# Kernel tuning notes

Hardware: AMD Instinct MI355X
Metric: run time of the kernel (lower is better)

## Reference

```python
import jax, jax.numpy as jnp
import numpy as np
import math

D_MODEL = 1024
NUM_HEADS = 16
HEAD_DIM = D_MODEL // NUM_HEADS


def setup_inputs() -> dict:
    key = jax.random.key(0)
    ks = jax.random.split(key, 9)
    B, S = 2, 2048
    scale = 1.0 / math.sqrt(D_MODEL)
    x = jax.random.normal(ks[0], (B, S, D_MODEL), dtype=jnp.float32)
    # torch nn.Linear params: weight [out, in], bias [out]
    Wq = jax.random.normal(ks[1], (D_MODEL, D_MODEL), dtype=jnp.float32) * scale
    bq = jax.random.normal(ks[2], (D_MODEL,), dtype=jnp.float32) * scale
    Wk = jax.random.normal(ks[3], (D_MODEL, D_MODEL), dtype=jnp.float32) * scale
    bk = jax.random.normal(ks[4], (D_MODEL,), dtype=jnp.float32) * scale
    Wv = jax.random.normal(ks[5], (D_MODEL, D_MODEL), dtype=jnp.float32) * scale
    bv = jax.random.normal(ks[6], (D_MODEL,), dtype=jnp.float32) * scale
    Wo = jax.random.normal(ks[7], (D_MODEL, D_MODEL), dtype=jnp.float32) * scale
    bo = jax.random.normal(ks[8], (D_MODEL,), dtype=jnp.float32) * scale
    return {"x": x, "Wq": Wq, "bq": bq, "Wk": Wk, "bk": bk,
            "Wv": Wv, "bv": bv, "Wo": Wo, "bo": bo}


def reference(x, Wq, bq, Wk, bk, Wv, bv, Wo, bo):
    B, S, _ = x.shape
    H, Dh = NUM_HEADS, HEAD_DIM

    def proj(W, b):
        # torch Linear: x @ W.T + b -> [B,S,D] -> [B,H,S,Dh]
        y = jnp.einsum('bsd,ed->bse', x, W) + b
        return y.reshape(B, S, H, Dh).transpose(0, 2, 1, 3)

    Q = proj(Wq, bq)
    K = proj(Wk, bk)
    V = proj(Wv, bv)

    # scores [B,H,S,S], causal mask with -inf, then scale by 1/sqrt(head_dim)
    scores = jnp.einsum('bhqd,bhkd->bhqk', Q, K)
    causal = jnp.tril(jnp.ones((S, S), dtype=bool))
    scores = jnp.where(causal, scores, -jnp.inf)
    A = jax.nn.softmax(scores / math.sqrt(Dh), axis=-1)

    O = jnp.einsum('bhqk,bhkd->bhqd', A, V)  # [B,H,S,Dh]
    O = O.transpose(0, 2, 1, 3).reshape(B, S, H * Dh)
    return jnp.einsum('bsd,ed->bse', O, Wo) + bo
```

## Files before the change

### kernel.cpp

```cpp
#include <hip/hip_runtime.h>


typedef _Float16 f16x8 __attribute__((ext_vector_type(8)));
typedef _Float16 f16x4 __attribute__((ext_vector_type(4)));
typedef _Float16 f16x2 __attribute__((ext_vector_type(2)));
typedef float f32x4 __attribute__((ext_vector_type(4)));

#define S_  2048
#define DM  1024
#define NH  16
#define DH  64

__device__ __forceinline__ void gload_lds16(const void* g, void* s) {
  __builtin_amdgcn_global_load_lds(
      (const __attribute__((address_space(1))) void*)g,
      (__attribute__((address_space(3))) void*)s, 16, 0, 0);
}

__device__ __forceinline__ f16x2 pkrtz(float a, float b) {
  return __builtin_bit_cast(f16x2, __builtin_amdgcn_cvt_pkrtz(a, b));
}


__global__ void cvt_x_kernel(const float* __restrict__ src,
                             _Float16* __restrict__ dst) {
  const int i = blockIdx.x * 256 + threadIdx.x;
  const float4 v = ((const float4*)src)[i];
  f16x4 h;
  h[0] = (_Float16)v.x; h[1] = (_Float16)v.y;
  h[2] = (_Float16)v.z; h[3] = (_Float16)v.w;
  ((f16x4*)dst)[i] = h;
}

__global__ void cvt_w_kernel(const float* __restrict__ w0,
                             const float* __restrict__ w1,
                             const float* __restrict__ w2,
                             const float* __restrict__ w3,
                             _Float16* __restrict__ dst) {
  const int y = blockIdx.y;
  const float* src = (y == 0) ? w0 : (y == 1) ? w1 : (y == 2) ? w2 : w3;
  const int i = blockIdx.x * 256 + threadIdx.x;
  const float4 v = ((const float4*)src)[i];
  f16x4 h;
  h[0] = (_Float16)v.x; h[1] = (_Float16)v.y;
  h[2] = (_Float16)v.z; h[3] = (_Float16)v.w;
  ((f16x4*)(dst + (size_t)y * (DM * DM)))[i] = h;
}


__global__ __launch_bounds__(256, 2) void gemm_qkv_kernel(
    const _Float16* __restrict__ xb, const _Float16* __restrict__ wb,
    const float* __restrict__ bq, const float* __restrict__ bk,
    const float* __restrict__ bv, _Float16* __restrict__ qkv)
{
  __shared__ _Float16 As[2][128 * 32];
  __shared__ _Float16 Ws[2][128 * 32];
  const int z = blockIdx.z;
  const _Float16* W = wb + (size_t)z * (DM * DM);
  const float* bias = (z == 0) ? bq : ((z == 1) ? bk : bv);
  _Float16* out = qkv + (size_t)z * 4194304;

  const f32x4 z4 = {0.f, 0.f, 0.f, 0.f};
  f32x4 acc[4][4];
#pragma unroll
  for (int mi = 0; mi < 4; ++mi)
#pragma unroll
    for (int ni = 0; ni < 4; ++ni) acc[mi][ni] = z4;

  const int m0 = blockIdx.y * 128, n0 = blockIdx.x * 128;
  const int t = threadIdx.x;
  const int w = t >> 6, l = t & 63;
  const int quad = l >> 4, ln = l & 15;
  const int wm = (w >> 1) << 6, wn = (w & 1) << 6;
  const int srow = l >> 2, scol = (l & 3) << 3;

  for (int k0 = 0; k0 < DM; k0 += 64) {
#pragma unroll
    for (int h = 0; h < 2; ++h)
#pragma unroll
      for (int i = 0; i < 2; ++i) {
        const int ra = w * 32 + i * 16;
        gload_lds16(&xb[(size_t)(m0 + ra + srow) * DM + k0 + h * 32 + scol],
                    &As[h][ra * 32]);
        gload_lds16(&W[(size_t)(n0 + ra + srow) * DM + k0 + h * 32 + scol],
                    &Ws[h][ra * 32]);
      }
    __syncthreads();

#pragma unroll
    for (int h = 0; h < 2; ++h) {
      f16x8 af[4], bf[4];
#pragma unroll
      for (int mi = 0; mi < 4; ++mi)
        af[mi] = *(const f16x8*)&As[h][(wm + mi * 16 + ln) * 32 + quad * 8];
#pragma unroll
      for (int ni = 0; ni < 4; ++ni)
        bf[ni] = *(const f16x8*)&Ws[h][(wn + ni * 16 + ln) * 32 + quad * 8];
#pragma unroll
      for (int mi = 0; mi < 4; ++mi)
#pragma unroll
        for (int ni = 0; ni < 4; ++ni)
          acc[mi][ni] = __builtin_amdgcn_mfma_f32_16x16x32_f16(
              af[mi], bf[ni], acc[mi][ni], 0, 0, 0);
    }
    __syncthreads();
  }

  const float scale = (z == 0) ? 0.18033688f : 1.0f;

#pragma unroll
  for (int ni = 0; ni < 4; ++ni) {
    const int c = n0 + wn + ni * 16 + ln;
    const float bias_c = bias[c];
    const int h = c >> 6, d = c & 63;
#pragma unroll
    for (int mi = 0; mi < 4; ++mi) {
      const int mb = m0 + wm + mi * 16 + quad * 4;
#pragma unroll
      for (int r = 0; r < 4; ++r) {
        const int mg = mb + r;
        const int b = mg >> 11, s = mg & 2047;
        const int bh = b * NH + h;
        const float v = (acc[mi][ni][r] + bias_c) * scale;
        size_t idx;
        if (z == 2)
          idx = (size_t)bh * 131072 + (s >> 5) * 2048 + (d >> 4) * 512 +
                ((s >> 3) & 3) * 128 + (d & 15) * 8 + (s & 7);
        else
          idx = (size_t)bh * 131072 + (s >> 4) * 1024 + (d >> 5) * 512 +
                ((d >> 3) & 3) * 128 + (s & 15) * 8 + (d & 7);
        out[idx] = (_Float16)v;
      }
    }
  }
}


__global__ __launch_bounds__(256, 2) void gemm_out_kernel(
    const _Float16* __restrict__ ob, const _Float16* __restrict__ wo,
    const float* __restrict__ bo, float* __restrict__ out)
{
  __shared__ _Float16 As[128 * 32];
  __shared__ _Float16 Ws[64 * 32];
  const f32x4 z4 = {0.f, 0.f, 0.f, 0.f};
  f32x4 acc[2][4];
#pragma unroll
  for (int mi = 0; mi < 2; ++mi)
#pragma unroll
    for (int ni = 0; ni < 4; ++ni) acc[mi][ni] = z4;

  const int m0 = blockIdx.y * 128, n0 = blockIdx.x * 64;
  const int t = threadIdx.x;
  const int w = t >> 6, l = t & 63;
  const int quad = l >> 4, ln = l & 15;
  const int srow = l >> 2, scol = (l & 3) << 3;

  for (int k0 = 0; k0 < DM; k0 += 32) {
#pragma unroll
    for (int i = 0; i < 2; ++i) {
      const int ra = w * 32 + i * 16;
      gload_lds16(&ob[(size_t)(m0 + ra + srow) * DM + k0 + scol], &As[ra * 32]);
    }
    gload_lds16(&wo[(size_t)(n0 + w * 16 + srow) * DM + k0 + scol],
                &Ws[w * 16 * 32]);
    __syncthreads();

    f16x8 af[2], bf[4];
#pragma unroll
    for (int mi = 0; mi < 2; ++mi)
      af[mi] = *(const f16x8*)&As[(w * 32 + mi * 16 + ln) * 32 + quad * 8];
#pragma unroll
    for (int ni = 0; ni < 4; ++ni)
      bf[ni] = *(const f16x8*)&Ws[(ni * 16 + ln) * 32 + quad * 8];
#pragma unroll
    for (int mi = 0; mi < 2; ++mi)
#pragma unroll
      for (int ni = 0; ni < 4; ++ni)
        acc[mi][ni] = __builtin_amdgcn_mfma_f32_16x16x32_f16(
            af[mi], bf[ni], acc[mi][ni], 0, 0, 0);
    __syncthreads();
  }

#pragma unroll
  for (int ni = 0; ni < 4; ++ni) {
    const int c = n0 + ni * 16 + ln;
    const float bias_c = bo[c];
#pragma unroll
    for (int mi = 0; mi < 2; ++mi) {
      const int mb = m0 + w * 32 + mi * 16 + quad * 4;
#pragma unroll
      for (int r = 0; r < 4; ++r)
        out[(size_t)(mb + r) * DM + c] = acc[mi][ni][r] + bias_c;
    }
  }
}


template <bool DIAG>
__device__ __forceinline__ void compute_tile(
    const _Float16* __restrict__ kb_, const _Float16* __restrict__ vb_,
    int t, const f16x8 (&qf)[2][2], f32x4 (&oacc)[4][2],
    float (&l_i)[2], _Float16* Ps, int quad, int ln, int l)
{
  f16x8 kf[4], vf[4];
#pragma unroll
  for (int i = 0; i < 4; ++i)
    kf[i] = *(const f16x8*)(kb_ + (size_t)(t * 4 + i) * 512 + l * 8);
#pragma unroll
  for (int i = 0; i < 4; ++i)
    vf[i] = *(const f16x8*)(vb_ + (size_t)(t * 4 + i) * 512 + l * 8);

  const f32x4 z4 = {0.f, 0.f, 0.f, 0.f};
  f32x4 sacc[2][2];
#pragma unroll
  for (int mi = 0; mi < 2; ++mi)
#pragma unroll
    for (int qc = 0; qc < 2; ++qc) sacc[mi][qc] = z4;

#pragma unroll
  for (int ks = 0; ks < 2; ++ks)
#pragma unroll
    for (int mi = 0; mi < 2; ++mi)
#pragma unroll
      for (int qc = 0; qc < 2; ++qc)
        sacc[mi][qc] = __builtin_amdgcn_mfma_f32_16x16x32_f16(
            kf[mi * 2 + ks], qf[qc][ks], sacc[mi][qc], 0, 0, 0);

  const int sw = (ln & 3) << 1;
#pragma unroll
  for (int qc = 0; qc < 2; ++qc) {
    float rs = 0.f;
#pragma unroll
    for (int mi = 0; mi < 2; ++mi) {
      float p[4];
#pragma unroll
      for (int r = 0; r < 4; ++r) {
        p[r] = __builtin_amdgcn_exp2f(sacc[mi][qc][r]);
        if (DIAG && (mi * 16 + quad * 4 + r > qc * 16 + ln)) p[r] = 0.f;
        rs += p[r];
      }
      const f16x2 lo = pkrtz(p[0], p[1]);
      const f16x2 hi = pkrtz(p[2], p[3]);
      const f16x4 pk = __builtin_shufflevector(lo, hi, 0, 1, 2, 3);
      const int g = (mi * 4 + quad) ^ sw;
      *(f16x4*)&Ps[(qc * 16 + ln) * 40 + g * 4] = pk;
    }
    l_i[qc] += rs;
  }

  f16x8 pb[2];
#pragma unroll
  for (int qc = 0; qc < 2; ++qc) {
    const int g2 = (quad * 2) ^ sw;
    pb[qc] = *(const f16x8*)&Ps[(qc * 16 + ln) * 40 + g2 * 4];
  }

#pragma unroll
  for (int di = 0; di < 4; ++di)
#pragma unroll
    for (int qc = 0; qc < 2; ++qc)
      oacc[di][qc] = __builtin_amdgcn_mfma_f32_16x16x32_f16(
          vf[di], pb[qc], oacc[di][qc], 0, 0, 0);
}

__global__ __launch_bounds__(256, 3) void attn_kernel(
    const _Float16* __restrict__ QF, const _Float16* __restrict__ KF,
    const _Float16* __restrict__ VF, _Float16* __restrict__ Ob)
{
  __shared__ _Float16 Ps[4 * 32 * 40];
  __shared__ float mrg[3 * 64 * 34];

  const int i = blockIdx.x;
  const int bh = ((i & 7) << 2) | ((i >> 3) & 3);
  const int p = i >> 5;

  const int tid = threadIdx.x;
  const int w = tid >> 6, l = tid & 63;
  const int quad = l >> 4, ln = l & 15;

  const _Float16* qb_ = QF + (size_t)bh * 131072;
  const _Float16* kb_ = KF + (size_t)bh * 131072;
  const _Float16* vb_ = VF + (size_t)bh * 131072;
  _Float16* psw = Ps + w * (32 * 40);
  const int bidx = bh >> 4, h = bh & 15;

  const f32x4 z4 = {0.f, 0.f, 0.f, 0.f};

#pragma unroll
  for (int mem = 0; mem < 2; ++mem) {
    const int qw = (mem == 0) ? (63 - p) : p;
    const int q0 = qw << 5;

    f16x8 qf[2][2];
#pragma unroll
    for (int qc = 0; qc < 2; ++qc)
#pragma unroll
      for (int ks = 0; ks < 2; ++ks)
        qf[qc][ks] = *(const f16x8*)
            (qb_ + (size_t)((2 * qw + qc) * 2 + ks) * 512 + l * 8);

    f32x4 oacc[4][2];
#pragma unroll
    for (int di = 0; di < 4; ++di)
#pragma unroll
      for (int qc = 0; qc < 2; ++qc) oacc[di][qc] = z4;
    float l_i[2] = {0.f, 0.f};

    int t = w;
    for (; t < qw; t += 4)
      compute_tile<false>(kb_, vb_, t, qf, oacc, l_i, psw, quad, ln, l);
    if (t == qw)
      compute_tile<true>(kb_, vb_, t, qf, oacc, l_i, psw, quad, ln, l);

#pragma unroll
    for (int qc = 0; qc < 2; ++qc) {
      float s = l_i[qc];
      s += __shfl_xor(s, 16);
      s += __shfl_xor(s, 32);
      l_i[qc] = s;
    }

    if (w != 0) {
      float* m_ = &mrg[((w - 1) * 64 + l) * 34];
#pragma unroll
      for (int di = 0; di < 4; ++di)
#pragma unroll
        for (int qc = 0; qc < 2; ++qc)
          *(f32x4*)(m_ + di * 8 + qc * 4) = oacc[di][qc];
      m_[32] = l_i[0];
      m_[33] = l_i[1];
    }
    __syncthreads();
    if (w == 0) {
#pragma unroll
      for (int ww = 0; ww < 3; ++ww) {
        const float* m_ = &mrg[(ww * 64 + l) * 34];
#pragma unroll
        for (int di = 0; di < 4; ++di)
#pragma unroll
          for (int qc = 0; qc < 2; ++qc)
            oacc[di][qc] += *(const f32x4*)(m_ + di * 8 + qc * 4);
        l_i[0] += m_[32];
        l_i[1] += m_[33];
      }
#pragma unroll
      for (int qc = 0; qc < 2; ++qc) {
        const float inv = 1.0f / l_i[qc];
        const int q = q0 + qc * 16 + ln;
        _Float16* orow = Ob + (size_t)(bidx * S_ + q) * DM + h * DH + quad * 4;
#pragma unroll
        for (int di = 0; di < 4; ++di) {
          f16x4 o4;
#pragma unroll
          for (int r = 0; r < 4; ++r)
            o4[r] = (_Float16)(oacc[di][qc][r] * inv);
          *(f16x4*)(orow + di * 16) = o4;
        }
      }
    }
    __syncthreads();
  }
}


extern "C" void kernel_launch(void* const* d_in, const int* in_sizes, int n_in,
                              void* d_out, int out_size, void* d_ws, size_t ws_size,
                              hipStream_t stream) {
  (void)in_sizes; (void)n_in; (void)out_size; (void)ws_size;
  const float* x  = (const float*)d_in[0];
  const float* Wq = (const float*)d_in[1];
  const float* bq = (const float*)d_in[2];
  const float* Wk = (const float*)d_in[3];
  const float* bk = (const float*)d_in[4];
  const float* Wv = (const float*)d_in[5];
  const float* bv = (const float*)d_in[6];
  const float* Wo = (const float*)d_in[7];
  const float* bo = (const float*)d_in[8];

  char* ws = (char*)d_ws;
  _Float16* xb  = (_Float16*)(ws);
  _Float16* wb  = (_Float16*)(ws + (8u << 20));
  _Float16* qkv = (_Float16*)(ws + (16u << 20));
  _Float16* ob  = (_Float16*)(ws + (40u << 20));

  cvt_x_kernel<<<dim3(4096), dim3(256), 0, stream>>>(x, xb);
  cvt_w_kernel<<<dim3(1024, 4), dim3(256), 0, stream>>>(Wq, Wk, Wv, Wo, wb);
  gemm_qkv_kernel<<<dim3(8, 32, 3), dim3(256), 0, stream>>>(xb, wb, bq, bk, bv, qkv);
  attn_kernel<<<dim3(1024), dim3(256), 0, stream>>>(
      qkv, qkv + 4194304, qkv + 2 * 4194304, ob);
  gemm_out_kernel<<<dim3(16, 32), dim3(256), 0, stream>>>(
      ob, wb + (size_t)3 * DM * DM, bo, (float*)d_out);
}
```

Baseline: 181.6 us.

## Merge conversion kernels, deepen out-GEMM K step, prefetch attention K tiles

The x and weight fp32-to-fp16 conversions are fused into a single launch, which removes one kernel launch. The output-projection GEMM now stages two 32-wide K slices per barrier pair, halving the number of __syncthreads round trips at the cost of doubled LDS. The attention inner loop software-prefetches the next K tile into registers while the current tile is computed, hiding global load latency but raising register pressure, which could hurt occupancy.

```diff
diff --git a/kernel.cpp b/kernel.cpp
--- a/kernel.cpp
+++ b/kernel.cpp
@@ -22,29 +22,31 @@
 }
 
 
-__global__ void cvt_x_kernel(const float* __restrict__ src,
-                             _Float16* __restrict__ dst) {
-  const int i = blockIdx.x * 256 + threadIdx.x;
-  const float4 v = ((const float4*)src)[i];
+__global__ void cvt_all_kernel(const float* __restrict__ x,
+                               const float* __restrict__ w0,
+                               const float* __restrict__ w1,
+                               const float* __restrict__ w2,
+                               const float* __restrict__ w3,
+                               _Float16* __restrict__ xb,
+                               _Float16* __restrict__ wb) {
+  const int bid = blockIdx.x;
+  const float* src;
+  _Float16* dst;
+  int idx;
+  if (bid < 4096) {
+    src = x; dst = xb; idx = bid * 256 + threadIdx.x;
+  } else {
+    const int j = bid - 4096;
+    const int y = j >> 10;
+    src = (y == 0) ? w0 : (y == 1) ? w1 : (y == 2) ? w2 : w3;
+    dst = wb + (size_t)y * (DM * DM);
+    idx = (j & 1023) * 256 + threadIdx.x;
+  }
+  const float4 v = ((const float4*)src)[idx];
   f16x4 h;
   h[0] = (_Float16)v.x; h[1] = (_Float16)v.y;
   h[2] = (_Float16)v.z; h[3] = (_Float16)v.w;
-  ((f16x4*)dst)[i] = h;
-}
-
-__global__ void cvt_w_kernel(const float* __restrict__ w0,
-                             const float* __restrict__ w1,
-                             const float* __restrict__ w2,
-                             const float* __restrict__ w3,
-                             _Float16* __restrict__ dst) {
-  const int y = blockIdx.y;
-  const float* src = (y == 0) ? w0 : (y == 1) ? w1 : (y == 2) ? w2 : w3;
-  const int i = blockIdx.x * 256 + threadIdx.x;
-  const float4 v = ((const float4*)src)[i];
-  f16x4 h;
-  h[0] = (_Float16)v.x; h[1] = (_Float16)v.y;
-  h[2] = (_Float16)v.z; h[3] = (_Float16)v.w;
-  ((f16x4*)(dst + (size_t)y * (DM * DM)))[i] = h;
+  ((f16x4*)dst)[idx] = h;
 }
 
 
@@ -140,8 +142,8 @@
     const _Float16* __restrict__ ob, const _Float16* __restrict__ wo,
     const float* __restrict__ bo, float* __restrict__ out)
 {
-  __shared__ _Float16 As[128 * 32];
-  __shared__ _Float16 Ws[64 * 32];
+  __shared__ _Float16 As[2][128 * 32];
+  __shared__ _Float16 Ws[2][64 * 32];
   const f32x4 z4 = {0.f, 0.f, 0.f, 0.f};
   f32x4 acc[2][4];
 #pragma unroll
@@ -155,29 +157,36 @@
   const int quad = l >> 4, ln = l & 15;
   const int srow = l >> 2, scol = (l & 3) << 3;
 
-  for (int k0 = 0; k0 < DM; k0 += 32) {
-#pragma unroll
-    for (int i = 0; i < 2; ++i) {
-      const int ra = w * 32 + i * 16;
-      gload_lds16(&ob[(size_t)(m0 + ra + srow) * DM + k0 + scol], &As[ra * 32]);
-    }
-    gload_lds16(&wo[(size_t)(n0 + w * 16 + srow) * DM + k0 + scol],
-                &Ws[w * 16 * 32]);
-    __syncthreads();
-
-    f16x8 af[2], bf[4];
-#pragma unroll
-    for (int mi = 0; mi < 2; ++mi)
-      af[mi] = *(const f16x8*)&As[(w * 32 + mi * 16 + ln) * 32 + quad * 8];
-#pragma unroll
-    for (int ni = 0; ni < 4; ++ni)
-      bf[ni] = *(const f16x8*)&Ws[(ni * 16 + ln) * 32 + quad * 8];
-#pragma unroll
-    for (int mi = 0; mi < 2; ++mi)
+  for (int k0 = 0; k0 < DM; k0 += 64) {
+#pragma unroll
+    for (int h = 0; h < 2; ++h) {
+#pragma unroll
+      for (int i = 0; i < 2; ++i) {
+        const int ra = w * 32 + i * 16;
+        gload_lds16(&ob[(size_t)(m0 + ra + srow) * DM + k0 + h * 32 + scol],
+                    &As[h][ra * 32]);
+      }
+      gload_lds16(&wo[(size_t)(n0 + w * 16 + srow) * DM + k0 + h * 32 + scol],
+                  &Ws[h][w * 16 * 32]);
+    }
+    __syncthreads();
+
+#pragma unroll
+    for (int h = 0; h < 2; ++h) {
+      f16x8 af[2], bf[4];
+#pragma unroll
+      for (int mi = 0; mi < 2; ++mi)
+        af[mi] = *(const f16x8*)&As[h][(w * 32 + mi * 16 + ln) * 32 + quad * 8];
 #pragma unroll
       for (int ni = 0; ni < 4; ++ni)
-        acc[mi][ni] = __builtin_amdgcn_mfma_f32_16x16x32_f16(
-            af[mi], bf[ni], acc[mi][ni], 0, 0, 0);
+        bf[ni] = *(const f16x8*)&Ws[h][(ni * 16 + ln) * 32 + quad * 8];
+#pragma unroll
+      for (int mi = 0; mi < 2; ++mi)
+#pragma unroll
+        for (int ni = 0; ni < 4; ++ni)
+          acc[mi][ni] = __builtin_amdgcn_mfma_f32_16x16x32_f16(
+              af[mi], bf[ni], acc[mi][ni], 0, 0, 0);
+    }
     __syncthreads();
   }
 
@@ -198,14 +207,11 @@
 
 template <bool DIAG>
 __device__ __forceinline__ void compute_tile(
-    const _Float16* __restrict__ kb_, const _Float16* __restrict__ vb_,
+    const f16x8 (&kf)[4], const _Float16* __restrict__ vb_,
     int t, const f16x8 (&qf)[2][2], f32x4 (&oacc)[4][2],
     float (&l_i)[2], _Float16* Ps, int quad, int ln, int l)
 {
-  f16x8 kf[4], vf[4];
-#pragma unroll
-  for (int i = 0; i < 4; ++i)
-    kf[i] = *(const f16x8*)(kb_ + (size_t)(t * 4 + i) * 512 + l * 8);
+  f16x8 vf[4];
 #pragma unroll
   for (int i = 0; i < 4; ++i)
     vf[i] = *(const f16x8*)(vb_ + (size_t)(t * 4 + i) * 512 + l * 8);
@@ -307,10 +313,26 @@
     float l_i[2] = {0.f, 0.f};
 
     int t = w;
-    for (; t < qw; t += 4)
-      compute_tile<false>(kb_, vb_, t, qf, oacc, l_i, psw, quad, ln, l);
-    if (t == qw)
-      compute_tile<true>(kb_, vb_, t, qf, oacc, l_i, psw, quad, ln, l);
+    if (t <= qw) {
+      f16x8 kf[4];
+#pragma unroll
+      for (int i2 = 0; i2 < 4; ++i2)
+        kf[i2] = *(const f16x8*)(kb_ + (size_t)(t * 4 + i2) * 512 + l * 8);
+      while (t + 4 <= qw) {
+        f16x8 kn[4];
+#pragma unroll
+        for (int i2 = 0; i2 < 4; ++i2)
+          kn[i2] = *(const f16x8*)(kb_ + (size_t)((t + 4) * 4 + i2) * 512 + l * 8);
+        compute_tile<false>(kf, vb_, t, qf, oacc, l_i, psw, quad, ln, l);
+#pragma unroll
+        for (int i2 = 0; i2 < 4; ++i2) kf[i2] = kn[i2];
+        t += 4;
+      }
+      if (t == qw)
+        compute_tile<true>(kf, vb_, t, qf, oacc, l_i, psw, quad, ln, l);
+      else
+        compute_tile<false>(kf, vb_, t, qf, oacc, l_i, psw, quad, ln, l);
+    }
 
 #pragma unroll
     for (int qc = 0; qc < 2; ++qc) {
@@ -383,8 +405,7 @@
   _Float16* qkv = (_Float16*)(ws + (16u << 20));
   _Float16* ob  = (_Float16*)(ws + (40u << 20));
 
-  cvt_x_kernel<<<dim3(4096), dim3(256), 0, stream>>>(x, xb);
-  cvt_w_kernel<<<dim3(1024, 4), dim3(256), 0, stream>>>(Wq, Wk, Wv, Wo, wb);
+  cvt_all_kernel<<<dim3(8192), dim3(256), 0, stream>>>(x, Wq, Wk, Wv, Wo, xb, wb);
   gemm_qkv_kernel<<<dim3(8, 32, 3), dim3(256), 0, stream>>>(xb, wb, bq, bk, bv, qkv);
   attn_kernel<<<dim3(1024), dim3(256), 0, stream>>>(
       qkv, qkv + 4194304, qkv + 2 * 4194304, ob);
```

Result: no change. 180.7 us (-0.5%).
